# Performance work log

Measured on AMD Instinct MI355X. Metric: run time of the kernel, lower is better.

## Reference

```python
import jax, jax.numpy as jnp
import numpy as np

N = 50000   # total nodes across batched graphs
E = 800000  # total edges
F = 30      # input node features
G = 256     # number of graphs in the disjoint batch
CH = [128, 64, 32]
N_LABELS = 2


def setup_inputs() -> dict:
    key = jax.random.key(0)
    ks = jax.random.split(key, 16)
    x = jax.random.normal(ks[0], (N, F), dtype=jnp.float32)
    edge_weight = jax.random.uniform(ks[1], (E,), dtype=jnp.float32)
    edge_row = jax.random.randint(ks[2], (E,), 0, N, dtype=jnp.int32)
    edge_col = jax.random.randint(ks[3], (E,), 0, N, dtype=jnp.int32)
    seg = jnp.sort(jax.random.randint(ks[4], (N,), 0, G, dtype=jnp.int32))
    # GCSConv params: out = A @ (x W1) + x W2 + b, per layer
    dims = [F] + CH
    params = {}
    kk = 5
    for l in range(3):
        fin, fout = dims[l], dims[l + 1]
        s = 1.0 / np.sqrt(fin)
        params[f"w1_{l+1}"] = jax.random.uniform(ks[kk], (fin, fout), minval=-s, maxval=s, dtype=jnp.float32); kk += 1
        params[f"w2_{l+1}"] = jax.random.uniform(ks[kk], (fin, fout), minval=-s, maxval=s, dtype=jnp.float32); kk += 1
        params[f"b_{l+1}"] = jnp.zeros((fout,), dtype=jnp.float32)
    sd = 1.0 / np.sqrt(CH[-1])
    params["wd"] = jax.random.uniform(ks[kk], (CH[-1], N_LABELS), minval=-sd, maxval=sd, dtype=jnp.float32)
    params["bd"] = jnp.zeros((N_LABELS,), dtype=jnp.float32)
    return {"x": x, "edge_weight": edge_weight, "edge_row": edge_row,
            "edge_col": edge_col, "seg": seg, **params}


def _gcs_conv(x, ew, er, ec, w1, w2, b):
    # spektral GCSConv: relu(A @ (x W1) + x W2 + b) with sparse A in COO form
    h = x @ w1                                   # [N, Fout]
    msgs = ew[:, None] * h[ec]                   # gather along edges [E, Fout]
    agg = jax.ops.segment_sum(msgs, er, num_segments=N)  # SpMM scatter [N, Fout]
    return jax.nn.relu(agg + x @ w2 + b)


def reference(x, edge_weight, edge_row, edge_col, seg,
              w1_1, w2_1, b_1, w1_2, w2_2, b_2, w1_3, w2_3, b_3, wd, bd):
    h = _gcs_conv(x, edge_weight, edge_row, edge_col, w1_1, w2_1, b_1)
    h = _gcs_conv(h, edge_weight, edge_row, edge_col, w1_2, w2_2, b_2)
    h = _gcs_conv(h, edge_weight, edge_row, edge_col, w1_3, w2_3, b_3)
    # GlobalAvgPool: segment mean over graph ids
    sums = jax.ops.segment_sum(h, seg, num_segments=G)               # [G, 32]
    cnts = jax.ops.segment_sum(jnp.ones((N,), h.dtype), seg, num_segments=G)
    pooled = sums / jnp.maximum(cnts, 1.0)[:, None]
    return jax.nn.softmax(pooled @ wd + bd, axis=-1)                 # [G, 2]
```

## Files before the change

### kernel.cpp

```cpp
#include <hip/hip_runtime.h>
#include <hip/hip_fp16.h>

#define N_NODES 50000
#define N_EDGES 800000
#define N_GRAPHS 256
#define NCB 196
#define CHUNK 3125
#define MBLK 782

typedef _Float16 f16x8 __attribute__((ext_vector_type(8)));
typedef float    f32x4 __attribute__((ext_vector_type(4)));

__global__ __launch_bounds__(256)
void hist_prep(const int* __restrict__ ER, const float* __restrict__ X,
               const int* __restrict__ SEG,
               const float* __restrict__ W1, const float* __restrict__ W2,
               const float* __restrict__ W12, const float* __restrict__ W22,
               const float* __restrict__ W13, const float* __restrict__ W23,
               int* __restrict__ ghist, __half* __restrict__ XPh,
               int* __restrict__ start,
               __half* __restrict__ W1f, __half* __restrict__ W2f,
               __half* __restrict__ W3f)
{
    int b = blockIdx.x;
    int t = threadIdx.x;
    if (b < 256) {
        __shared__ int h[NCB];
        for (int i = t; i < NCB; i += 256) h[i] = 0;
        __syncthreads();
        int lo = b * CHUNK, hi = lo + CHUNK;
        for (int e = lo + t; e < hi; e += 256) atomicAdd(&h[ER[e] >> 8], 1);
        __syncthreads();
        for (int i = t; i < NCB; i += 256) ghist[i * 256 + b] = h[i];
        return;
    }
    int bid = b - 256;
    if (bid < 6250) {
        int idx = bid * 256 + t;
        int n = idx >> 5;
        int c = idx & 31;
        float v = (c < 30) ? X[n * 30 + c] : 0.f;
        XPh[(size_t)n * 32 + c] = __float2half(v);
    } else if (bid < 6446) {
        int n = (bid - 6250) * 256 + t;
        if (n >= N_NODES) return;
        int g = SEG[n];
        int gprev = (n == 0) ? -1 : SEG[n - 1];
        for (int gg = gprev + 1; gg <= g; ++gg) start[gg] = n;
        if (n == N_NODES - 1)
            for (int gg = g + 1; gg <= N_GRAPHS; ++gg) start[gg] = N_NODES;
    } else {
        int idx = (bid - 6446) * 256 + t;
        if (idx < 8192) {
            int i = idx & 7, c = (idx >> 3) & 15, g = (idx >> 7) & 3;
            int s = (idx >> 9) & 1, n = idx >> 10;
            int k = s * 32 + g * 8 + i, col = n * 16 + c;
            float w = 0.f;
            if (k < 30) w = W1[k * 128 + col];
            else if (k >= 32 && k < 62) w = W2[(k - 32) * 128 + col];
            W1f[idx] = __float2half(w);
        } else if (idx < 24576) {
            int o = idx - 8192;
            int i = o & 7, c = (o >> 3) & 15, g = (o >> 7) & 3;
            int s = (o >> 9) & 3, n = o >> 11;
            int k = s * 32 + g * 8 + i, col = n * 16 + c;
            float w = (col < 64) ? W12[k * 64 + col] : W22[k * 64 + col - 64];
            W2f[o] = __float2half(w);
        } else {
            int o = idx - 24576;
            int i = o & 7, c = (o >> 3) & 15, g = (o >> 7) & 3;
            int s = (o >> 9) & 1, n = o >> 10;
            int k = s * 32 + g * 8 + i, col = n * 16 + c;
            float w = (col < 32) ? W13[k * 32 + col] : W23[k * 32 + col - 32];
            W3f[o] = __float2half(w);
        }
    }
}

__global__ __launch_bounds__(256)
void scan1(int* __restrict__ ghist, int* __restrict__ bsum)
{
    __shared__ int s[256];
    int t = threadIdx.x, b = blockIdx.x;
    int i = b * 256 + t;
    int v = ghist[i];
    s[t] = v;
    __syncthreads();
    for (int off = 1; off < 256; off <<= 1) {
        int u = (t >= off) ? s[t - off] : 0;
        __syncthreads();
        s[t] += u;
        __syncthreads();
    }
    ghist[i] = s[t] - v;
    if (t == 255) bsum[b] = s[255];
}

__global__ __launch_bounds__(256)
void c_scatter(const int* __restrict__ ER, const int* __restrict__ EC,
               const float* __restrict__ EW, const int* __restrict__ ghist,
               const int* __restrict__ bsum, unsigned int* __restrict__ tmp_sd,
               __half* __restrict__ tmp_w)
{
    __shared__ int s[256];
    __shared__ int cur[NCB];
    int t = threadIdx.x, blk = blockIdx.x;
    int v = (t < NCB) ? bsum[t] : 0;
    s[t] = v;
    __syncthreads();
    for (int off = 1; off < 256; off <<= 1) {
        int u = (t >= off) ? s[t - off] : 0;
        __syncthreads();
        s[t] += u;
        __syncthreads();
    }
    if (t < NCB) cur[t] = (s[t] - v) + ghist[t * 256 + blk];
    __syncthreads();
    int lo = blk * CHUNK, hi = lo + CHUNK;
    for (int e = lo + t; e < hi; e += 256) {
        int d = ER[e];
        int pos = atomicAdd(&cur[d >> 8], 1);
        tmp_sd[pos] = (unsigned int)EC[e] | ((unsigned int)(d & 255) << 16);
        tmp_w[pos] = __float2half(EW[e]);
    }
}

__device__ __forceinline__ void fma8h(float4& a0, float4& a1, float w,
                                      const uint4& raw)
{
    const __half2* hp = (const __half2*)&raw;
    float2 f0 = __half22float2(hp[0]);
    float2 f1 = __half22float2(hp[1]);
    float2 f2 = __half22float2(hp[2]);
    float2 f3 = __half22float2(hp[3]);
    a0.x = fmaf(w, f0.x, a0.x); a0.y = fmaf(w, f0.y, a0.y);
    a0.z = fmaf(w, f1.x, a0.z); a0.w = fmaf(w, f1.y, a0.w);
    a1.x = fmaf(w, f2.x, a1.x); a1.y = fmaf(w, f2.y, a1.y);
    a1.z = fmaf(w, f3.x, a1.z); a1.w = fmaf(w, f3.y, a1.w);
}

__device__ __forceinline__ unsigned int relu2(unsigned int u)
{
    unsigned int lo = (u & 0x8000u)     ? 0u : (u & 0x0000FFFFu);
    unsigned int hi = (u & 0x80000000u) ? 0u : (u & 0xFFFF0000u);
    return lo | hi;
}

__global__ __launch_bounds__(1024)
void bsort_aggx(const unsigned int* __restrict__ tmp_sd, const __half* __restrict__ tmp_w,
                const int* __restrict__ bsum, const __half* __restrict__ XPh,
                unsigned int* __restrict__ packed, int* __restrict__ rowptr,
                __half* __restrict__ CIa)
{
    __shared__ int s[256];
    __shared__ int hist[256];
    __shared__ int cur[256];
    __shared__ int r0arr[257];
    int t = threadIdx.x, b = blockIdx.x;

    if (t < 256) s[t] = (t < NCB) ? bsum[t] : 0;
    __syncthreads();
    for (int off = 1; off < 256; off <<= 1) {
        int u = 0;
        if (t < 256 && t >= off) u = s[t - off];
        __syncthreads();
        if (t < 256) s[t] += u;
        __syncthreads();
    }
    int cntb = bsum[b];
    int base = s[b] - cntb;
    int end  = base + cntb;
    __syncthreads();

    if (t < 256) hist[t] = 0;
    __syncthreads();
    for (int j = base + t; j < end; j += 1024)
        atomicAdd(&hist[(tmp_sd[j] >> 16) & 255], 1);
    __syncthreads();
    int hv = 0;
    if (t < 256) { hv = hist[t]; s[t] = hv; }
    __syncthreads();
    for (int off = 1; off < 256; off <<= 1) {
        int u = 0;
        if (t < 256 && t >= off) u = s[t - off];
        __syncthreads();
        if (t < 256) s[t] += u;
        __syncthreads();
    }
    if (t < 256) {
        int excl = s[t] - hv;
        int n = b * 256 + t;
        if (n < N_NODES) rowptr[n] = base + excl;
        if (b == NCB - 1 && t == 0) rowptr[N_NODES] = N_EDGES;
        r0arr[t] = base + excl;
        cur[t] = base + excl;
        if (t == 0) r0arr[256] = end;
    }
    __syncthreads();
    for (int j = base + t; j < end; j += 1024) {
        unsigned int sd = tmp_sd[j];
        unsigned short hb = __half_as_ushort(tmp_w[j]);
        int pos = atomicAdd(&cur[(sd >> 16) & 255], 1);
        packed[pos] = (sd & 0xFFFF) | ((unsigned int)hb << 16);
    }
    __syncthreads();

    {
        int local = t >> 2;
        int q = t & 3;
        int n = b * 256 + local;
        if (n < N_NODES) {
            int r0 = r0arr[local], r1 = r0arr[local + 1];
            float4 acc0 = make_float4(0.f, 0.f, 0.f, 0.f);
            float4 acc1 = make_float4(0.f, 0.f, 0.f, 0.f);
            int j = r0;
            for (; j + 3 < r1; j += 4) {
                unsigned int ra = packed[j],     rb = packed[j + 1];
                unsigned int rc = packed[j + 2], rd = packed[j + 3];
                uint4 rawa = *(const uint4*)(XPh + (size_t)(ra & 0xFFFF) * 32 + q * 8);
                uint4 rawb = *(const uint4*)(XPh + (size_t)(rb & 0xFFFF) * 32 + q * 8);
                uint4 rawc = *(const uint4*)(XPh + (size_t)(rc & 0xFFFF) * 32 + q * 8);
                uint4 rawd = *(const uint4*)(XPh + (size_t)(rd & 0xFFFF) * 32 + q * 8);
                float wa = __half2float(__ushort_as_half((unsigned short)(ra >> 16)));
                float wb = __half2float(__ushort_as_half((unsigned short)(rb >> 16)));
                float wc = __half2float(__ushort_as_half((unsigned short)(rc >> 16)));
                float wd = __half2float(__ushort_as_half((unsigned short)(rd >> 16)));
                fma8h(acc0, acc1, wa, rawa);
                fma8h(acc0, acc1, wb, rawb);
                fma8h(acc0, acc1, wc, rawc);
                fma8h(acc0, acc1, wd, rawd);
            }
            for (; j < r1; ++j) {
                unsigned int r = packed[j];
                uint4 raw = *(const uint4*)(XPh + (size_t)(r & 0xFFFF) * 32 + q * 8);
                float w = __half2float(__ushort_as_half((unsigned short)(r >> 16)));
                fma8h(acc0, acc1, w, raw);
            }
            __half2 hb2[4];
            hb2[0] = __float22half2_rn(make_float2(acc0.x, acc0.y));
            hb2[1] = __float22half2_rn(make_float2(acc0.z, acc0.w));
            hb2[2] = __float22half2_rn(make_float2(acc1.x, acc1.y));
            hb2[3] = __float22half2_rn(make_float2(acc1.z, acc1.w));
            *(uint4*)(CIa + (size_t)n * 32 + q * 8) = *(uint4*)&hb2[0];
        }
    }
}

__global__ __launch_bounds__(256)
void dense12_mfma(const __half* __restrict__ CIa, const __half* __restrict__ XPh,
                  const __half* __restrict__ W1f, const float* __restrict__ B1,
                  const __half* __restrict__ W2f, const float* __restrict__ B2,
                  __half* __restrict__ H2h, __half* __restrict__ A2h)
{
    __shared__ __align__(16) __half As[64 * 72];
    __shared__ __align__(16) __half Hs[64 * 136];
    const int tid = threadIdx.x;
    const int m0 = blockIdx.x * 64;
    const int lane = tid & 63;
    const int w  = tid >> 6;
    const int lr = lane & 15;
    const int lg = lane >> 4;

    for (int idx = tid; idx < 512; idx += 256) {
        int row = idx >> 3, c8 = idx & 7;
        int gm = m0 + row;
        uint4 v = make_uint4(0, 0, 0, 0);
        if (gm < N_NODES) {
            const __half* src = (c8 < 4) ? (CIa + (size_t)gm * 32 + c8 * 8)
                                         : (XPh + (size_t)gm * 32 + (c8 - 4) * 8);
            v = *(const uint4*)src;
        }
        *(uint4*)(As + row * 72 + c8 * 8) = v;
    }
    __syncthreads();

    f32x4 acc[4][2];
    #pragma unroll
    for (int m = 0; m < 4; ++m)
        #pragma unroll
        for (int j = 0; j < 2; ++j)
            acc[m][j] = (f32x4){0.f, 0.f, 0.f, 0.f};

    #pragma unroll
    for (int s = 0; s < 2; ++s) {
        f16x8 a[4];
        #pragma unroll
        for (int m = 0; m < 4; ++m)
            a[m] = *(const f16x8*)(As + (m * 16 + lr) * 72 + s * 32 + lg * 8);
        #pragma unroll
        for (int j = 0; j < 2; ++j) {
            const int n = 2 * w + j;
            f16x8 b = *(const f16x8*)(W1f + (((n * 2 + s) * 4 + lg) * 16 + lr) * 8);
            #pragma unroll
            for (int m = 0; m < 4; ++m)
                acc[m][j] = __builtin_amdgcn_mfma_f32_16x16x32_f16(a[m], b, acc[m][j], 0, 0, 0);
        }
    }

    #pragma unroll
    for (int j = 0; j < 2; ++j) {
        const int n = 2 * w + j;
        const float bias = B1[n * 16 + lr];
        #pragma unroll
        for (int m = 0; m < 4; ++m)
            #pragma unroll
            for (int r = 0; r < 4; ++r) {
                float v = fmaxf(acc[m][j][r] + bias, 0.f);
                Hs[(m * 16 + lg * 4 + r) * 136 + n * 16 + lr] = __float2half(v);
            }
    }
    __syncthreads();

    f32x4 acc2[4][2];
    #pragma unroll
    for (int m = 0; m < 4; ++m)
        #pragma unroll
        for (int j = 0; j < 2; ++j)
            acc2[m][j] = (f32x4){0.f, 0.f, 0.f, 0.f};

    #pragma unroll
    for (int s = 0; s < 4; ++s) {
        f16x8 a[4];
        #pragma unroll
        for (int m = 0; m < 4; ++m)
            a[m] = *(const f16x8*)(Hs + (m * 16 + lr) * 136 + s * 32 + lg * 8);
        #pragma unroll
        for (int j = 0; j < 2; ++j) {
            const int n = 2 * w + j;
            f16x8 b = *(const f16x8*)(W2f + (((n * 4 + s) * 4 + lg) * 16 + lr) * 8);
            #pragma unroll
            for (int m = 0; m < 4; ++m)
                acc2[m][j] = __builtin_amdgcn_mfma_f32_16x16x32_f16(a[m], b, acc2[m][j], 0, 0, 0);
        }
    }
    __syncthreads();

    #pragma unroll
    for (int j = 0; j < 2; ++j) {
        const int n = 2 * w + j;
        const float bias = (n >= 4) ? B2[(n - 4) * 16 + lr] : 0.f;
        #pragma unroll
        for (int m = 0; m < 4; ++m)
            #pragma unroll
            for (int r = 0; r < 4; ++r)
                Hs[(m * 16 + lg * 4 + r) * 136 + n * 16 + lr] =
                    __float2half(acc2[m][j][r] + bias);
    }
    __syncthreads();

    for (int idx = tid; idx < 1024; idx += 256) {
        int row = idx >> 4, c8 = idx & 15;
        int gm = m0 + row;
        if (gm < N_NODES) {
            uint4 v = *(const uint4*)(Hs + row * 136 + c8 * 8);
            if (c8 < 8) *(uint4*)(H2h + (size_t)gm * 64 + c8 * 8) = v;
            else        *(uint4*)(A2h + (size_t)gm * 64 + (c8 - 8) * 8) = v;
        }
    }
}

__global__ __launch_bounds__(256)
void dense3_mfma(const __half* __restrict__ X, const __half* __restrict__ W3f,
                 const float* __restrict__ B3, __half* __restrict__ H3h,
                 __half* __restrict__ B2h)
{
    __shared__ __align__(16) __half As[64 * 72];
    __shared__ __align__(16) __half Os[64 * 72];
    const int tid = threadIdx.x;
    const int m0 = blockIdx.x * 64;
    const int lane = tid & 63;
    const int w  = tid >> 6;
    const int lr = lane & 15;
    const int lg = lane >> 4;

    for (int idx = tid; idx < 512; idx += 256) {
        int row = idx >> 3, c8 = idx & 7;
        int gm = m0 + row;
        uint4 v = make_uint4(0, 0, 0, 0);
        if (gm < N_NODES) v = *(const uint4*)(X + (size_t)gm * 64 + c8 * 8);
        v.x = relu2(v.x); v.y = relu2(v.y); v.z = relu2(v.z); v.w = relu2(v.w);
        *(uint4*)(As + row * 72 + c8 * 8) = v;
    }
    __syncthreads();

    f32x4 acc[4];
    #pragma unroll
    for (int m = 0; m < 4; ++m) acc[m] = (f32x4){0.f, 0.f, 0.f, 0.f};

    #pragma unroll
    for (int s = 0; s < 2; ++s) {
        f16x8 b = *(const f16x8*)(W3f + (((w * 2 + s) * 4 + lg) * 16 + lr) * 8);
        #pragma unroll
        for (int m = 0; m < 4; ++m) {
            f16x8 a = *(const f16x8*)(As + (m * 16 + lr) * 72 + s * 32 + lg * 8);
            acc[m] = __builtin_amdgcn_mfma_f32_16x16x32_f16(a, b, acc[m], 0, 0, 0);
        }
    }

    const float bias = (w >= 2) ? B3[(w - 2) * 16 + lr] : 0.f;
    #pragma unroll
    for (int m = 0; m < 4; ++m)
        #pragma unroll
        for (int r = 0; r < 4; ++r)
            Os[(m * 16 + lg * 4 + r) * 72 + w * 16 + lr] =
                __float2half(acc[m][r] + bias);
    __syncthreads();

    for (int idx = tid; idx < 512; idx += 256) {
        int row = idx >> 3, c8 = idx & 7;
        int gm = m0 + row;
        if (gm < N_NODES) {
            uint4 v = *(const uint4*)(Os + row * 72 + c8 * 8);
            if (c8 < 4) *(uint4*)(H3h + (size_t)gm * 32 + c8 * 8) = v;
            else        *(uint4*)(B2h + (size_t)gm * 32 + (c8 - 4) * 8) = v;
        }
    }
}

template<int FOUT>
__global__ __launch_bounds__(512)
void spmm_split(const __half* __restrict__ H, const int* __restrict__ rowptr,
                const unsigned int* __restrict__ packed, __half* __restrict__ AGGh)
{
    constexpr int T = FOUT / 8;
    constexpr int NPB = 512 / (2 * T);
    __shared__ float part[NPB][FOUT + 4];
    int tid = threadIdx.x;
    int local = tid / (2 * T);
    int rem = tid % (2 * T);
    int s = rem / T;
    int q = rem % T;
    int n = blockIdx.x * NPB + local;
    bool valid = (n < N_NODES);
    float4 acc0 = make_float4(0.f, 0.f, 0.f, 0.f);
    float4 acc1 = make_float4(0.f, 0.f, 0.f, 0.f);
    __half* ap = AGGh + (size_t)n * FOUT + q * 8;
    if (valid) {
        int r0 = rowptr[n], r1 = rowptr[n + 1];
        int mid = (r0 + r1) >> 1;
        int lo = s ? mid : r0;
        int hi = s ? r1 : mid;
        if (s == 0) {
            uint4 raw = *(const uint4*)ap;
            const __half2* hp = (const __half2*)&raw;
            float2 f0 = __half22float2(hp[0]);
            float2 f1 = __half22float2(hp[1]);
            float2 f2 = __half22float2(hp[2]);
            float2 f3 = __half22float2(hp[3]);
            acc0 = make_float4(f0.x, f0.y, f1.x, f1.y);
            acc1 = make_float4(f2.x, f2.y, f3.x, f3.y);
        }
        int j = lo;
        for (; j + 3 < hi; j += 4) {
            unsigned int ra = packed[j],     rb = packed[j + 1];
            unsigned int rc = packed[j + 2], rd = packed[j + 3];
            uint4 rawa = *(const uint4*)(H + (size_t)(ra & 0xFFFF) * FOUT + q * 8);
            uint4 rawb = *(const uint4*)(H + (size_t)(rb & 0xFFFF) * FOUT + q * 8);
            uint4 rawc = *(const uint4*)(H + (size_t)(rc & 0xFFFF) * FOUT + q * 8);
            uint4 rawd = *(const uint4*)(H + (size_t)(rd & 0xFFFF) * FOUT + q * 8);
            float wa = __half2float(__ushort_as_half((unsigned short)(ra >> 16)));
            float wb = __half2float(__ushort_as_half((unsigned short)(rb >> 16)));
            float wc = __half2float(__ushort_as_half((unsigned short)(rc >> 16)));
            float wd = __half2float(__ushort_as_half((unsigned short)(rd >> 16)));
            fma8h(acc0, acc1, wa, rawa);
            fma8h(acc0, acc1, wb, rawb);
            fma8h(acc0, acc1, wc, rawc);
            fma8h(acc0, acc1, wd, rawd);
        }
        for (; j < hi; ++j) {
            unsigned int r = packed[j];
            uint4 raw = *(const uint4*)(H + (size_t)(r & 0xFFFF) * FOUT + q * 8);
            float w = __half2float(__ushort_as_half((unsigned short)(r >> 16)));
            fma8h(acc0, acc1, w, raw);
        }
    }
    if (s == 1) {
        *(float4*)&part[local][q * 8 + 0] = acc0;
        *(float4*)&part[local][q * 8 + 4] = acc1;
    }
    __syncthreads();
    if (s == 0 && valid) {
        float4 p0 = *(float4*)&part[local][q * 8 + 0];
        float4 p1 = *(float4*)&part[local][q * 8 + 4];
        acc0.x += p0.x; acc0.y += p0.y; acc0.z += p0.z; acc0.w += p0.w;
        acc1.x += p1.x; acc1.y += p1.y; acc1.z += p1.z; acc1.w += p1.w;
        __half2 hb[4];
        hb[0] = __float22half2_rn(make_float2(acc0.x, acc0.y));
        hb[1] = __float22half2_rn(make_float2(acc0.z, acc0.w));
        hb[2] = __float22half2_rn(make_float2(acc1.x, acc1.y));
        hb[3] = __float22half2_rn(make_float2(acc1.z, acc1.w));
        *(uint4*)ap = *(uint4*)&hb[0];
    }
}

__global__ __launch_bounds__(256)
void pool_kernel(const __half* __restrict__ H, const int* __restrict__ start,
                 const float* __restrict__ WD, const float* __restrict__ BD,
                 float* __restrict__ OUT)
{
    __shared__ float red[8][33];
    int g = blockIdx.x;
    int s = start[g], e = start[g + 1];
    int q = threadIdx.x & 31;
    int lane = threadIdx.x >> 5;
    float acc = 0.f;
    for (int n = s + lane; n < e; n += 8)
        acc += fmaxf(__half2float(H[(size_t)n * 32 + q]), 0.f);
    red[lane][q] = acc;
    __syncthreads();
    if (threadIdx.x < 32) {
        float v = 0.f;
        #pragma unroll
        for (int i = 0; i < 8; ++i) v += red[i][q];
        float inv = (e > s) ? 1.0f / (float)(e - s) : 1.0f;
        float p = v * inv;
        float p0 = p * WD[q * 2 + 0];
        float p1 = p * WD[q * 2 + 1];
        #pragma unroll
        for (int off = 16; off; off >>= 1) {
            p0 += __shfl_down(p0, off, 32);
            p1 += __shfl_down(p1, off, 32);
        }
        if (q == 0) {
            float l0 = p0 + BD[0], l1 = p1 + BD[1];
            float m = fmaxf(l0, l1);
            float e0 = expf(l0 - m), e1 = expf(l1 - m);
            float si = 1.0f / (e0 + e1);
            OUT[g * 2 + 0] = e0 * si;
            OUT[g * 2 + 1] = e1 * si;
        }
    }
}

extern "C" void kernel_launch(void* const* d_in, const int* in_sizes, int n_in,
                              void* d_out, int out_size, void* d_ws, size_t ws_size,
                              hipStream_t stream)
{
    const float* x    = (const float*)d_in[0];
    const float* ew   = (const float*)d_in[1];
    const int*   er   = (const int*)d_in[2];
    const int*   ec   = (const int*)d_in[3];
    const int*   seg  = (const int*)d_in[4];
    const float* w1_1 = (const float*)d_in[5];
    const float* w2_1 = (const float*)d_in[6];
    const float* b_1  = (const float*)d_in[7];
    const float* w1_2 = (const float*)d_in[8];
    const float* w2_2 = (const float*)d_in[9];
    const float* b_2  = (const float*)d_in[10];
    const float* w1_3 = (const float*)d_in[11];
    const float* w2_3 = (const float*)d_in[12];
    const float* b_3  = (const float*)d_in[13];
    const float* wd   = (const float*)d_in[14];
    const float* bd   = (const float*)d_in[15];

    float* ws = (float*)d_ws;
    int*   IW = (int*)d_ws;
    __half* XPh    = (__half*)ws;
    __half* CIa    = (__half*)(ws + 800000);
    unsigned int* tmp_sd = (unsigned int*)(ws + 1600000);
    __half* tmp_w  = (__half*)(ws + 2400000);
    __half* H2h    = (__half*)(ws + 3200000);
    __half* A2h    = (__half*)(ws + 4800000);
    __half* H3h    = (__half*)(ws + 6400000);
    __half* B2h    = (__half*)(ws + 7200000);
    unsigned int* packed = (unsigned int*)(IW + 8000000);
    int*    rowptr = IW + 9000000;
    int*    ghist  = IW + 9060000;
    int*    bsum   = IW + 9115000;
    int*    start  = IW + 9120000;
    __half* W1f    = (__half*)(ws + 9125000);
    __half* W2f    = (__half*)(ws + 9130000);
    __half* W3f    = (__half*)(ws + 9139000);

    dim3 blk(256);

    hist_prep<<<dim3(256 + 6558), blk, 0, stream>>>(er, x, seg, w1_1, w2_1,
                                                    w1_2, w2_2, w1_3, w2_3,
                                                    ghist, XPh, start,
                                                    W1f, W2f, W3f);
    scan1<<<dim3(NCB), blk, 0, stream>>>(ghist, bsum);
    c_scatter<<<dim3(256), blk, 0, stream>>>(er, ec, ew, ghist, bsum, tmp_sd, tmp_w);
    bsort_aggx<<<dim3(NCB), dim3(1024), 0, stream>>>(tmp_sd, tmp_w, bsum, XPh,
                                                     packed, rowptr, CIa);

    dense12_mfma<<<dim3(MBLK), blk, 0, stream>>>(CIa, XPh, W1f, b_1,
                                                 W2f, b_2, H2h, A2h);
    spmm_split<64><<<dim3((N_NODES + 31) / 32), dim3(512), 0, stream>>>(H2h, rowptr,
                                                                        packed, A2h);
    dense3_mfma<<<dim3(MBLK), blk, 0, stream>>>(A2h, W3f, b_3, H3h, B2h);
    spmm_split<32><<<dim3(MBLK), dim3(512), 0, stream>>>(H3h, rowptr, packed, B2h);

    pool_kernel<<<dim3(N_GRAPHS), blk, 0, stream>>>(B2h, start, wd, bd, (float*)d_out);
}
```

Measured before the change: 176.7 us.

## Fuse layer-1 edge aggregation into dense MFMA kernel, widen SpMM and pool splits

The layer-1 gather-aggregation moves out of the sort kernel and into the first dense MFMA kernel, which now reads rowptr and packed and writes the aggregated features straight into shared memory. This drops the CIa intermediate buffer round trip and lets the 1024-thread sort kernel finish sooner. The SpMM kernel is generalized to split each row's edge range S ways, now 4 instead of 2, reducing per-thread serial work at the cost of more shared-memory partial sums. The pool kernel also moves to 1024 threads per graph.

```diff
diff --git a/kernel.cpp b/kernel.cpp
--- a/kernel.cpp
+++ b/kernel.cpp
@@ -147,15 +147,13 @@
 }
 
 __global__ __launch_bounds__(1024)
-void bsort_aggx(const unsigned int* __restrict__ tmp_sd, const __half* __restrict__ tmp_w,
-                const int* __restrict__ bsum, const __half* __restrict__ XPh,
-                unsigned int* __restrict__ packed, int* __restrict__ rowptr,
-                __half* __restrict__ CIa)
+void bsort(const unsigned int* __restrict__ tmp_sd, const __half* __restrict__ tmp_w,
+           const int* __restrict__ bsum,
+           unsigned int* __restrict__ packed, int* __restrict__ rowptr)
 {
     __shared__ int s[256];
     __shared__ int hist[256];
     __shared__ int cur[256];
-    __shared__ int r0arr[257];
     int t = threadIdx.x, b = blockIdx.x;
 
     if (t < 256) s[t] = (t < NCB) ? bsum[t] : 0;
@@ -192,9 +190,7 @@
         int n = b * 256 + t;
         if (n < N_NODES) rowptr[n] = base + excl;
         if (b == NCB - 1 && t == 0) rowptr[N_NODES] = N_EDGES;
-        r0arr[t] = base + excl;
         cur[t] = base + excl;
-        if (t == 0) r0arr[256] = end;
     }
     __syncthreads();
     for (int j = base + t; j < end; j += 1024) {
@@ -203,14 +199,37 @@
         int pos = atomicAdd(&cur[(sd >> 16) & 255], 1);
         packed[pos] = (sd & 0xFFFF) | ((unsigned int)hb << 16);
     }
-    __syncthreads();
+}
+
+__global__ __launch_bounds__(256)
+void dense12_mfma(const __half* __restrict__ XPh, const int* __restrict__ rowptr,
+                  const unsigned int* __restrict__ packed,
+                  const __half* __restrict__ W1f, const float* __restrict__ B1,
+                  const __half* __restrict__ W2f, const float* __restrict__ B2,
+                  __half* __restrict__ H2h, __half* __restrict__ A2h)
+{
+    __shared__ __align__(16) __half As[64 * 72];
+    __shared__ __align__(16) __half Hs[64 * 136];
+    const int tid = threadIdx.x;
+    const int m0 = blockIdx.x * 64;
+    const int lane = tid & 63;
+    const int w  = tid >> 6;
+    const int lr = lane & 15;
+    const int lg = lane >> 4;
 
     {
-        int local = t >> 2;
-        int q = t & 3;
-        int n = b * 256 + local;
+        int row = tid >> 2, c4 = tid & 3;
+        int gm = m0 + row;
+        uint4 v = make_uint4(0, 0, 0, 0);
+        if (gm < N_NODES) v = *(const uint4*)(XPh + (size_t)gm * 32 + c4 * 8);
+        *(uint4*)(As + row * 72 + (4 + c4) * 8) = v;
+    }
+    {
+        int local = tid >> 2, q = tid & 3;
+        int n = m0 + local;
+        __half2 hb2[4];
         if (n < N_NODES) {
-            int r0 = r0arr[local], r1 = r0arr[local + 1];
+            int r0 = rowptr[n], r1 = rowptr[n + 1];
             float4 acc0 = make_float4(0.f, 0.f, 0.f, 0.f);
             float4 acc1 = make_float4(0.f, 0.f, 0.f, 0.f);
             int j = r0;
@@ -233,44 +252,17 @@
             for (; j < r1; ++j) {
                 unsigned int r = packed[j];
                 uint4 raw = *(const uint4*)(XPh + (size_t)(r & 0xFFFF) * 32 + q * 8);
-                float w = __half2float(__ushort_as_half((unsigned short)(r >> 16)));
-                fma8h(acc0, acc1, w, raw);
+                float wv = __half2float(__ushort_as_half((unsigned short)(r >> 16)));
+                fma8h(acc0, acc1, wv, raw);
             }
-            __half2 hb2[4];
             hb2[0] = __float22half2_rn(make_float2(acc0.x, acc0.y));
             hb2[1] = __float22half2_rn(make_float2(acc0.z, acc0.w));
             hb2[2] = __float22half2_rn(make_float2(acc1.x, acc1.y));
             hb2[3] = __float22half2_rn(make_float2(acc1.z, acc1.w));
-            *(uint4*)(CIa + (size_t)n * 32 + q * 8) = *(uint4*)&hb2[0];
-        }
-    }
-}
-
-__global__ __launch_bounds__(256)
-void dense12_mfma(const __half* __restrict__ CIa, const __half* __restrict__ XPh,
-                  const __half* __restrict__ W1f, const float* __restrict__ B1,
-                  const __half* __restrict__ W2f, const float* __restrict__ B2,
-                  __half* __restrict__ H2h, __half* __restrict__ A2h)
-{
-    __shared__ __align__(16) __half As[64 * 72];
-    __shared__ __align__(16) __half Hs[64 * 136];
-    const int tid = threadIdx.x;
-    const int m0 = blockIdx.x * 64;
-    const int lane = tid & 63;
-    const int w  = tid >> 6;
-    const int lr = lane & 15;
-    const int lg = lane >> 4;
-
-    for (int idx = tid; idx < 512; idx += 256) {
-        int row = idx >> 3, c8 = idx & 7;
-        int gm = m0 + row;
-        uint4 v = make_uint4(0, 0, 0, 0);
-        if (gm < N_NODES) {
-            const __half* src = (c8 < 4) ? (CIa + (size_t)gm * 32 + c8 * 8)
-                                         : (XPh + (size_t)gm * 32 + (c8 - 4) * 8);
-            v = *(const uint4*)src;
-        }
-        *(uint4*)(As + row * 72 + c8 * 8) = v;
+        } else {
+            hb2[0] = hb2[1] = hb2[2] = hb2[3] = __float22half2_rn(make_float2(0.f, 0.f));
+        }
+        *(uint4*)(As + local * 72 + q * 8) = *(uint4*)&hb2[0];
     }
     __syncthreads();
 
@@ -417,17 +409,17 @@
     }
 }
 
-template<int FOUT>
+template<int FOUT, int S>
 __global__ __launch_bounds__(512)
 void spmm_split(const __half* __restrict__ H, const int* __restrict__ rowptr,
                 const unsigned int* __restrict__ packed, __half* __restrict__ AGGh)
 {
     constexpr int T = FOUT / 8;
-    constexpr int NPB = 512 / (2 * T);
-    __shared__ float part[NPB][FOUT + 4];
+    constexpr int NPB = 512 / (S * T);
+    __shared__ float part[NPB][S - 1][FOUT + 4];
     int tid = threadIdx.x;
-    int local = tid / (2 * T);
-    int rem = tid % (2 * T);
+    int local = tid / (S * T);
+    int rem = tid % (S * T);
     int s = rem / T;
     int q = rem % T;
     int n = blockIdx.x * NPB + local;
@@ -437,9 +429,9 @@
     __half* ap = AGGh + (size_t)n * FOUT + q * 8;
     if (valid) {
         int r0 = rowptr[n], r1 = rowptr[n + 1];
-        int mid = (r0 + r1) >> 1;
-        int lo = s ? mid : r0;
-        int hi = s ? r1 : mid;
+        int deg = r1 - r0;
+        int lo = r0 + (deg * s) / S;
+        int hi = r0 + (deg * (s + 1)) / S;
         if (s == 0) {
             uint4 raw = *(const uint4*)ap;
             const __half2* hp = (const __half2*)&raw;
@@ -474,16 +466,19 @@
             fma8h(acc0, acc1, w, raw);
         }
     }
-    if (s == 1) {
-        *(float4*)&part[local][q * 8 + 0] = acc0;
-        *(float4*)&part[local][q * 8 + 4] = acc1;
+    if (s > 0) {
+        *(float4*)&part[local][s - 1][q * 8 + 0] = acc0;
+        *(float4*)&part[local][s - 1][q * 8 + 4] = acc1;
     }
     __syncthreads();
     if (s == 0 && valid) {
-        float4 p0 = *(float4*)&part[local][q * 8 + 0];
-        float4 p1 = *(float4*)&part[local][q * 8 + 4];
-        acc0.x += p0.x; acc0.y += p0.y; acc0.z += p0.z; acc0.w += p0.w;
-        acc1.x += p1.x; acc1.y += p1.y; acc1.z += p1.z; acc1.w += p1.w;
+        #pragma unroll
+        for (int ss = 0; ss < S - 1; ++ss) {
+            float4 p0 = *(float4*)&part[local][ss][q * 8 + 0];
+            float4 p1 = *(float4*)&part[local][ss][q * 8 + 4];
+            acc0.x += p0.x; acc0.y += p0.y; acc0.z += p0.z; acc0.w += p0.w;
+            acc1.x += p1.x; acc1.y += p1.y; acc1.z += p1.z; acc1.w += p1.w;
+        }
         __half2 hb[4];
         hb[0] = __float22half2_rn(make_float2(acc0.x, acc0.y));
         hb[1] = __float22half2_rn(make_float2(acc0.z, acc0.w));
@@ -493,25 +488,25 @@
     }
 }
 
-__global__ __launch_bounds__(256)
+__global__ __launch_bounds__(1024)
 void pool_kernel(const __half* __restrict__ H, const int* __restrict__ start,
                  const float* __restrict__ WD, const float* __restrict__ BD,
                  float* __restrict__ OUT)
 {
-    __shared__ float red[8][33];
+    __shared__ float red[32][33];
     int g = blockIdx.x;
     int s = start[g], e = start[g + 1];
     int q = threadIdx.x & 31;
-    int lane = threadIdx.x >> 5;
+    int grp = threadIdx.x >> 5;
     float acc = 0.f;
-    for (int n = s + lane; n < e; n += 8)
+    for (int n = s + grp; n < e; n += 32)
         acc += fmaxf(__half2float(H[(size_t)n * 32 + q]), 0.f);
-    red[lane][q] = acc;
+    red[grp][q] = acc;
     __syncthreads();
     if (threadIdx.x < 32) {
         float v = 0.f;
         #pragma unroll
-        for (int i = 0; i < 8; ++i) v += red[i][q];
+        for (int i = 0; i < 32; ++i) v += red[i][q];
         float inv = (e > s) ? 1.0f / (float)(e - s) : 1.0f;
         float p = v * inv;
         float p0 = p * WD[q * 2 + 0];
@@ -556,7 +551,6 @@
     float* ws = (float*)d_ws;
     int*   IW = (int*)d_ws;
     __half* XPh    = (__half*)ws;
-    __half* CIa    = (__half*)(ws + 800000);
     unsigned int* tmp_sd = (unsigned int*)(ws + 1600000);
     __half* tmp_w  = (__half*)(ws + 2400000);
     __half* H2h    = (__half*)(ws + 3200000);
@@ -580,15 +574,16 @@
                                                     W1f, W2f, W3f);
     scan1<<<dim3(NCB), blk, 0, stream>>>(ghist, bsum);
     c_scatter<<<dim3(256), blk, 0, stream>>>(er, ec, ew, ghist, bsum, tmp_sd, tmp_w);
-    bsort_aggx<<<dim3(NCB), dim3(1024), 0, stream>>>(tmp_sd, tmp_w, bsum, XPh,
-                                                     packed, rowptr, CIa);
-
-    dense12_mfma<<<dim3(MBLK), blk, 0, stream>>>(CIa, XPh, W1f, b_1,
+    bsort<<<dim3(NCB), dim3(1024), 0, stream>>>(tmp_sd, tmp_w, bsum, packed, rowptr);
+
+    dense12_mfma<<<dim3(MBLK), blk, 0, stream>>>(XPh, rowptr, packed, W1f, b_1,
                                                  W2f, b_2, H2h, A2h);
-    spmm_split<64><<<dim3((N_NODES + 31) / 32), dim3(512), 0, stream>>>(H2h, rowptr,
-                                                                        packed, A2h);
+    spmm_split<64, 4><<<dim3((N_NODES + 15) / 16), dim3(512), 0, stream>>>(H2h, rowptr,
+                                                                           packed, A2h);
     dense3_mfma<<<dim3(MBLK), blk, 0, stream>>>(A2h, W3f, b_3, H3h, B2h);
-    spmm_split<32><<<dim3(MBLK), dim3(512), 0, stream>>>(H3h, rowptr, packed, B2h);
-
-    pool_kernel<<<dim3(N_GRAPHS), blk, 0, stream>>>(B2h, start, wd, bd, (float*)d_out);
-}
+    spmm_split<32, 4><<<dim3((N_NODES + 31) / 32), dim3(512), 0, stream>>>(H3h, rowptr,
+                                                                           packed, B2h);
+
+    pool_kernel<<<dim3(N_GRAPHS), dim3(1024), 0, stream>>>(B2h, start, wd, bd,
+                                                           (float*)d_out);
+}
```

Measured after the change: 174.7 us. About the same (-1.2%).
